# Performance work log

Measured on AMD Instinct MI355X. Metric: run time of the kernel, lower is better.

The kernel has to match this reference:

```python
import jax, jax.numpy as jnp
import numpy as np

# ---- config constants (from ResidualNetConfig) ----
BOUND_LO = jnp.array([-5.0, -5.0, -5.0], dtype=jnp.float32)
BOUND_DIS = jnp.array([10.0, 10.0, 10.0], dtype=jnp.float32)
N_MIN = 200                 # int(ceil(max extent)/resolution) = 10/0.05
PER_LEVEL_SCALE = 2.0
NUM_LEVELS = 4
LOG2_T = 19
T = 1 << LOG2_T
OUTPUT_SDF_SCALE = 0.1
LEAKY_SLOPE = 0.01

# Instant-NGP spatial hash primes (first coord uses 1)
PRIMES = (np.uint32(1), np.uint32(2654435761), np.uint32(805459861))
# 8 corner offsets of the unit cube, [8, 3]
CORNERS = jnp.array([[(c >> d) & 1 for d in range(3)] for c in range(8)], dtype=jnp.uint32)


def hash_grid_encode(xyz01, tables):
    """xyz01: [N,3] in [0,1]; tables: [L,T,F] -> [N, L*F] trilinear hashed features."""
    feats = []
    for l in range(NUM_LEVELS):
        res = jnp.float32(N_MIN * (PER_LEVEL_SCALE ** l))
        pos = xyz01 * res                       # [N,3]
        pfloor = jnp.floor(pos)
        frac = pos - pfloor                     # [N,3]
        base = pfloor.astype(jnp.uint32)        # [N,3]
        corner = base[:, None, :] + CORNERS[None, :, :]   # [N,8,3]
        h = (corner[..., 0] * PRIMES[0]) ^ (corner[..., 1] * PRIMES[1]) ^ (corner[..., 2] * PRIMES[2])
        idx = (h & jnp.uint32(T - 1)).astype(jnp.int32)   # [N,8]
        f = tables[l][idx]                      # [N,8,F] irregular gather
        # trilinear weights: prod over dims of frac (corner=1) or 1-frac (corner=0)
        w = jnp.prod(jnp.where(CORNERS[None].astype(bool), frac[:, None, :], 1.0 - frac[:, None, :]), axis=-1)  # [N,8]
        feats.append(jnp.sum(f * w[..., None], axis=1))   # [N,F]
    return jnp.concatenate(feats, axis=-1)      # [N, L*F]


def leaky_relu(x):
    return jnp.where(x >= 0, x, LEAKY_SLOPE * x)


def setup_inputs() -> dict:
    key = jax.random.key(0)
    k1, k2, k3, k4, k5 = jax.random.split(key, 5)
    N = 2_000_000
    xyz = jax.random.uniform(k1, (N, 3), dtype=jnp.float32) * BOUND_DIS + BOUND_LO
    tables = jax.random.normal(k2, (NUM_LEVELS, T, 2), dtype=jnp.float32) * 1e-2
    W_in = jax.random.normal(k3, (8, 64), dtype=jnp.float32) / np.sqrt(8.0)
    W_h = jax.random.normal(k4, (64, 64), dtype=jnp.float32) / np.sqrt(64.0)
    W_out = jax.random.normal(k5, (64, 1), dtype=jnp.float32) / np.sqrt(64.0)
    return {"xyz": xyz, "tables": tables, "W_in": W_in, "W_h": W_h, "W_out": W_out}


def reference(xyz, tables, W_in, W_h, W_out):
    # scale_with_bound: map xyz into [0,1]^3
    xyz01 = (xyz - BOUND_LO) / BOUND_DIS
    enc = hash_grid_encode(xyz01, tables)        # [N, 8]
    h = leaky_relu(enc @ W_in)                   # hidden layer 1
    h = leaky_relu(h @ W_h)                      # hidden layer 2
    sdf = (h @ W_out).reshape(-1) * OUTPUT_SDF_SCALE
    return sdf
```

## Files before the change

### kernel.cpp

```cpp
#include <hip/hip_runtime.h>
#include <hip/hip_fp16.h>

static constexpr unsigned TSIZE = 1u << 19;
static constexpr unsigned TMASK = TSIZE - 1u;

typedef _Float16 f16;
typedef f16   f16x8 __attribute__((ext_vector_type(8)));
typedef float f32x4 __attribute__((ext_vector_type(4)));

union H2U { __half2 h; unsigned u; };

__global__ __launch_bounds__(256)
void cvt_tables(const float4* __restrict__ in, __half2* __restrict__ out, int n4)
{
    int i = blockIdx.x * 256 + threadIdx.x;
    if (i < n4) {
        float4 v = in[i];
        out[2 * i]     = __floats2half2_rn(v.x, v.y);
        out[2 * i + 1] = __floats2half2_rn(v.z, v.w);
    }
}

__device__ __forceinline__ void hash_level(float px, float py, float pz, int l,
                                           const __half2* __restrict__ tab,
                                           float& e0, float& e1)
{
    const float res = 200.0f * (float)(1 << l);
    const float fx = px * res, fy = py * res, fz = pz * res;
    const float flx = floorf(fx), fly = floorf(fy), flz = floorf(fz);
    const float frx = fx - flx, fry = fy - fly, frz = fz - flz;
    const unsigned bx = (unsigned)flx, by = (unsigned)fly, bz = (unsigned)flz;
    const unsigned hy0 = by * 2654435761u, hy1 = (by + 1u) * 2654435761u;
    const unsigned hz0 = bz * 805459861u,  hz1 = (bz + 1u) * 805459861u;
    const float wx[2] = {1.0f - frx, frx};
    const float wy[2] = {1.0f - fry, fry};
    const float wz[2] = {1.0f - frz, frz};
    e0 = 0.0f; e1 = 0.0f;
    #pragma unroll
    for (int c = 0; c < 8; ++c) {
        unsigned h = (bx + (unsigned)(c & 1))
                   ^ ((c & 2) ? hy1 : hy0)
                   ^ ((c & 4) ? hz1 : hz0);
        __half2 fv = tab[h & TMASK];
        float2 f = __half22float2(fv);
        float w = wx[c & 1] * wy[(c >> 1) & 1] * wz[(c >> 2) & 1];
        e0 = fmaf(f.x, w, e0);
        e1 = fmaf(f.y, w, e1);
    }
}

__device__ __forceinline__ void stage_xyz(const float* __restrict__ xyz, int bbase, int N,
                                          float* sxyz, float& px, float& py, float& pz)
{
    const int g3 = bbase * 3;
    #pragma unroll
    for (int t = 0; t < 3; ++t) {
        int sidx = (int)threadIdx.x + t * 256;
        int g = g3 + sidx;
        sxyz[sidx] = (g < 3 * N) ? __builtin_nontemporal_load(&xyz[g]) : 0.0f;
    }
    __syncthreads();
    px = (sxyz[threadIdx.x * 3 + 0] + 5.0f) * 0.1f;
    py = (sxyz[threadIdx.x * 3 + 1] + 5.0f) * 0.1f;
    pz = (sxyz[threadIdx.x * 3 + 2] + 5.0f) * 0.1f;
}

__global__ __launch_bounds__(256, 8)
void encode01(const float* __restrict__ xyz, const __half2* __restrict__ tab16,
              unsigned long long* __restrict__ enc01, int N)
{
    __shared__ float sxyz[768];
    const int bbase = blockIdx.x * 256;
    const int i = bbase + (int)threadIdx.x;
    float px, py, pz;
    stage_xyz(xyz, bbase, N, sxyz, px, py, pz);

    float e0, e1, e2, e3;
    hash_level(px, py, pz, 0, tab16,         e0, e1);
    hash_level(px, py, pz, 1, tab16 + TSIZE, e2, e3);

    H2U a, b;
    a.h = __floats2half2_rn(e0, e1);
    b.h = __floats2half2_rn(e2, e3);
    if (i < N) {
        unsigned long long v = (unsigned long long)a.u
                             | ((unsigned long long)b.u << 32);
        __builtin_nontemporal_store(v, &enc01[i]);
    }
}

static constexpr int H1_STRIDE = 72;

__global__ __launch_bounds__(256, 2)
void mlp23_mfma(const float* __restrict__ xyz, const __half2* __restrict__ tab16,
                const unsigned long long* __restrict__ enc01,
                const float* __restrict__ Win, const float* __restrict__ Wh,
                const float* __restrict__ Wout, float* __restrict__ out, int N)
{
    __shared__ float sxyz[768];
    __shared__ f16 h1s[256 * H1_STRIDE];

    const int bbase = blockIdx.x * 256;
    const int i = bbase + (int)threadIdx.x;
    float px, py, pz;
    stage_xyz(xyz, bbase, N, sxyz, px, py, pz);

    float enc[8];
    {
        unsigned long long v = __builtin_nontemporal_load(&enc01[i < N ? i : 0]);
        H2U a, b; a.u = (unsigned)v; b.u = (unsigned)(v >> 32);
        float2 f01 = __half22float2(a.h);
        float2 f23 = __half22float2(b.h);
        enc[0] = f01.x; enc[1] = f01.y; enc[2] = f23.x; enc[3] = f23.y;
    }
    hash_level(px, py, pz, 2, tab16 + 2 * TSIZE, enc[4], enc[5]);
    hash_level(px, py, pz, 3, tab16 + 3 * TSIZE, enc[6], enc[7]);

    float h1[64];
    #pragma unroll
    for (int j = 0; j < 64; ++j) h1[j] = 0.0f;
    #pragma unroll
    for (int k = 0; k < 8; ++k) {
        const float e = enc[k];
        #pragma unroll
        for (int j = 0; j < 64; ++j)
            h1[j] = fmaf(e, Win[k * 64 + j], h1[j]);
    }
    {
        f16* row = &h1s[(int)threadIdx.x * H1_STRIDE];
        #pragma unroll
        for (int jj = 0; jj < 8; ++jj) {
            f16x8 v;
            #pragma unroll
            for (int e = 0; e < 8; ++e) {
                float a = h1[jj * 8 + e];
                a = (a >= 0.0f) ? a : 0.01f * a;
                v[e] = (f16)a;
            }
            *(f16x8*)(row + jj * 8) = v;
        }
    }
    __syncthreads();

    const int wave = (int)threadIdx.x >> 6;
    const int lane = (int)threadIdx.x & 63;
    const int c = lane & 15;
    const int q = lane >> 4;
    const f16* wbase = &h1s[wave * 64 * H1_STRIDE];

    f16x8 bfrag[2][4];
    #pragma unroll
    for (int kt = 0; kt < 2; ++kt)
        #pragma unroll
        for (int nt = 0; nt < 4; ++nt)
            #pragma unroll
            for (int j = 0; j < 8; ++j)
                bfrag[kt][nt][j] = (f16)Wh[(kt * 32 + q * 8 + j) * 64 + nt * 16 + c];

    f32x4 Ct[4][4];
    #pragma unroll
    for (int mt = 0; mt < 4; ++mt)
        #pragma unroll
        for (int nt = 0; nt < 4; ++nt)
            Ct[mt][nt] = (f32x4){0.f, 0.f, 0.f, 0.f};

    #pragma unroll
    for (int mt = 0; mt < 4; ++mt) {
        #pragma unroll
        for (int kt = 0; kt < 2; ++kt) {
            const f16x8 a = *(const f16x8*)&wbase[(mt * 16 + c) * H1_STRIDE + kt * 32 + q * 8];
            #pragma unroll
            for (int nt = 0; nt < 4; ++nt)
                Ct[mt][nt] = __builtin_amdgcn_mfma_f32_16x16x32_f16(a, bfrag[kt][nt], Ct[mt][nt], 0, 0, 0);
        }
    }

    float acc3[4][4];
    #pragma unroll
    for (int mt = 0; mt < 4; ++mt)
        #pragma unroll
        for (int r = 0; r < 4; ++r) acc3[mt][r] = 0.0f;

    #pragma unroll
    for (int nt = 0; nt < 4; ++nt) {
        const float wo = Wout[nt * 16 + c];
        #pragma unroll
        for (int mt = 0; mt < 4; ++mt)
            #pragma unroll
            for (int r = 0; r < 4; ++r) {
                float v = Ct[mt][nt][r];
                v = (v >= 0.0f) ? v : 0.01f * v;
                acc3[mt][r] = fmaf(v, wo, acc3[mt][r]);
            }
    }
    #pragma unroll
    for (int mask = 1; mask <= 8; mask <<= 1)
        #pragma unroll
        for (int mt = 0; mt < 4; ++mt)
            #pragma unroll
            for (int r = 0; r < 4; ++r)
                acc3[mt][r] += __shfl_xor(acc3[mt][r], mask, 64);

    if (c == 0) {
        #pragma unroll
        for (int mt = 0; mt < 4; ++mt)
            #pragma unroll
            for (int r = 0; r < 4; ++r) {
                int p = bbase + wave * 64 + mt * 16 + q * 4 + r;
                if (p < N) out[p] = acc3[mt][r] * 0.1f;
            }
    }
}

__global__ __launch_bounds__(256, 2)
void resnet_mono(const float* __restrict__ xyz, const float* __restrict__ tables,
                 const float* __restrict__ Win, const float* __restrict__ Wh,
                 const float* __restrict__ Wout, float* __restrict__ out, int N)
{
    __shared__ float sxyz[768];
    const int bbase = blockIdx.x * 256;
    const int i = bbase + (int)threadIdx.x;
    float px, py, pz;
    stage_xyz(xyz, bbase, N, sxyz, px, py, pz);

    float enc[8];
    #pragma unroll
    for (int l = 0; l < 4; ++l) {
        const float res = 200.0f * (float)(1 << l);
        const float fx = px * res, fy = py * res, fz = pz * res;
        const float flx = floorf(fx), fly = floorf(fy), flz = floorf(fz);
        const float frx = fx - flx, fry = fy - fly, frz = fz - flz;
        const unsigned bx = (unsigned)flx, by = (unsigned)fly, bz = (unsigned)flz;
        const unsigned hy0 = by * 2654435761u, hy1 = (by + 1u) * 2654435761u;
        const unsigned hz0 = bz * 805459861u,  hz1 = (bz + 1u) * 805459861u;
        const float wx[2] = {1.0f - frx, frx};
        const float wy[2] = {1.0f - fry, fry};
        const float wz[2] = {1.0f - frz, frz};
        const float2* tab = (const float2*)tables + (size_t)l * TSIZE;
        float e0 = 0.0f, e1 = 0.0f;
        #pragma unroll
        for (int cc = 0; cc < 8; ++cc) {
            unsigned h = (bx + (unsigned)(cc & 1))
                       ^ ((cc & 2) ? hy1 : hy0)
                       ^ ((cc & 4) ? hz1 : hz0);
            float2 f = tab[h & TMASK];
            float w = wx[cc & 1] * wy[(cc >> 1) & 1] * wz[(cc >> 2) & 1];
            e0 = fmaf(f.x, w, e0);
            e1 = fmaf(f.y, w, e1);
        }
        enc[2 * l] = e0; enc[2 * l + 1] = e1;
    }

    float h1[64];
    #pragma unroll
    for (int j = 0; j < 64; ++j) h1[j] = 0.0f;
    #pragma unroll
    for (int k = 0; k < 8; ++k) {
        const float e = enc[k];
        #pragma unroll
        for (int j = 0; j < 64; ++j)
            h1[j] = fmaf(e, Win[k * 64 + j], h1[j]);
    }
    #pragma unroll
    for (int j = 0; j < 64; ++j)
        h1[j] = (h1[j] >= 0.0f) ? h1[j] : 0.01f * h1[j];

    float sdf = 0.0f;
    #pragma unroll
    for (int j0 = 0; j0 < 64; j0 += 16) {
        float acc[16];
        #pragma unroll
        for (int jj = 0; jj < 16; ++jj) acc[jj] = 0.0f;
        #pragma unroll
        for (int k = 0; k < 64; ++k) {
            const float hk = h1[k];
            #pragma unroll
            for (int jj = 0; jj < 16; ++jj)
                acc[jj] = fmaf(hk, Wh[k * 64 + j0 + jj], acc[jj]);
        }
        #pragma unroll
        for (int jj = 0; jj < 16; ++jj) {
            float a = acc[jj];
            a = (a >= 0.0f) ? a : 0.01f * a;
            sdf = fmaf(a, Wout[j0 + jj], sdf);
        }
    }
    if (i < N) out[i] = sdf * 0.1f;
}

extern "C" void kernel_launch(void* const* d_in, const int* in_sizes, int n_in,
                              void* d_out, int out_size, void* d_ws, size_t ws_size,
                              hipStream_t stream) {
    const float* xyz    = (const float*)d_in[0];
    const float* tables = (const float*)d_in[1];
    const float* Win    = (const float*)d_in[2];
    const float* Wh     = (const float*)d_in[3];
    const float* Wout   = (const float*)d_in[4];
    float* out = (float*)d_out;

    const int N = in_sizes[0] / 3;
    const int blocks = (N + 255) / 256;

    const int tab_floats = in_sizes[1];
    const size_t tab16_bytes = (size_t)tab_floats * 2;
    const size_t enc01_bytes = (size_t)N * 8;

    if (ws_size >= tab16_bytes + enc01_bytes) {
        __half2* tab16 = (__half2*)d_ws;
        unsigned long long* enc01 = (unsigned long long*)((char*)d_ws + tab16_bytes);
        int n4 = tab_floats / 4;
        hipLaunchKernelGGL(cvt_tables, dim3((n4 + 255) / 256), dim3(256), 0, stream,
                           (const float4*)tables, tab16, n4);
        hipLaunchKernelGGL(encode01, dim3(blocks), dim3(256), 0, stream,
                           xyz, tab16, enc01, N);
        hipLaunchKernelGGL(mlp23_mfma, dim3(blocks), dim3(256), 0, stream,
                           xyz, tab16, enc01, Win, Wh, Wout, out, N);
    } else {
        hipLaunchKernelGGL(resnet_mono, dim3(blocks), dim3(256), 0, stream,
                           xyz, tables, Win, Wh, Wout, out, N);
    }
}
```

Baseline: 324.6 us.

## Pair hash-grid corner gathers into 8-byte loads and issue all levels before blending

Within each level, corners c and c+1 differ only in x. When bx is even, their hashed indices (bx^s) and ((bx+1)^s) are adjacent, so one aligned uint2 load fetches both. When bx is odd, four extra single loads fetch the second corner. All gathers for both levels, plus the enc01 load, are now issued before any blending, which exposes memory-level parallelism. Launch bounds change to 4 blocks per SM for both kernels, and the intent is to cut the number of scattered gather instructions and overlap their latency. The cost is more live registers, a divergent branch when bx parity differs across lanes, and occupancy that changes in opposite directions for the two kernels.

Result: no change. 328.7 us (+1.3%).

```diff
diff --git a/kernel.cpp b/kernel.cpp
--- a/kernel.cpp
+++ b/kernel.cpp
@@ -21,31 +21,66 @@
     }
 }
 
-__device__ __forceinline__ void hash_level(float px, float py, float pz, int l,
-                                           const __half2* __restrict__ tab,
-                                           float& e0, float& e1)
-{
+struct HashIssue {
+    uint2    pv[4];
+    unsigned uodd[4];
+    unsigned flags;
+    float    frx, fry, frz;
+};
+
+__device__ __forceinline__ HashIssue hash_issue(float px, float py, float pz, int l,
+                                                const __half2* __restrict__ tab)
+{
+    HashIssue r;
     const float res = 200.0f * (float)(1 << l);
     const float fx = px * res, fy = py * res, fz = pz * res;
     const float flx = floorf(fx), fly = floorf(fy), flz = floorf(fz);
-    const float frx = fx - flx, fry = fy - fly, frz = fz - flz;
+    r.frx = fx - flx; r.fry = fy - fly; r.frz = fz - flz;
     const unsigned bx = (unsigned)flx, by = (unsigned)fly, bz = (unsigned)flz;
     const unsigned hy0 = by * 2654435761u, hy1 = (by + 1u) * 2654435761u;
     const unsigned hz0 = bz * 805459861u,  hz1 = (bz + 1u) * 805459861u;
-    const float wx[2] = {1.0f - frx, frx};
-    const float wy[2] = {1.0f - fry, fry};
-    const float wz[2] = {1.0f - frz, frz};
+    const unsigned syz[4] = { hy0 ^ hz0, hy1 ^ hz0, hy0 ^ hz1, hy1 ^ hz1 };
+    const uint2* __restrict__ tabp = (const uint2*)tab;
+
+    unsigned flags = (bx & 1u) << 4;
+    #pragma unroll
+    for (int p = 0; p < 4; ++p) {
+        const unsigned i0 = (bx ^ syz[p]) & TMASK;
+        r.pv[p] = tabp[i0 >> 1];
+        flags |= (i0 & 1u) << p;
+        r.uodd[p] = 0u;
+    }
+    if (bx & 1u) {
+        #pragma unroll
+        for (int p = 0; p < 4; ++p) {
+            const unsigned i1 = ((bx + 1u) ^ syz[p]) & TMASK;
+            H2U t; t.h = tab[i1];
+            r.uodd[p] = t.u;
+        }
+    }
+    r.flags = flags;
+    return r;
+}
+
+__device__ __forceinline__ void hash_blend(const HashIssue& r, float& e0, float& e1)
+{
+    const float wx0 = 1.0f - r.frx, wx1 = r.frx;
+    const float wyv[2] = {1.0f - r.fry, r.fry};
+    const float wzv[2] = {1.0f - r.frz, r.frz};
+    const bool bxodd = (r.flags >> 4) & 1u;
     e0 = 0.0f; e1 = 0.0f;
     #pragma unroll
-    for (int c = 0; c < 8; ++c) {
-        unsigned h = (bx + (unsigned)(c & 1))
-                   ^ ((c & 2) ? hy1 : hy0)
-                   ^ ((c & 4) ? hz1 : hz0);
-        __half2 fv = tab[h & TMASK];
-        float2 f = __half22float2(fv);
-        float w = wx[c & 1] * wy[(c >> 1) & 1] * wz[(c >> 2) & 1];
-        e0 = fmaf(f.x, w, e0);
-        e1 = fmaf(f.y, w, e1);
+    for (int p = 0; p < 4; ++p) {
+        const bool sw = (r.flags >> p) & 1u;
+        unsigned a = sw ? r.pv[p].y : r.pv[p].x;
+        unsigned b = sw ? r.pv[p].x : r.pv[p].y;
+        b = bxodd ? r.uodd[p] : b;
+        H2U ua, ub; ua.u = a; ub.u = b;
+        const float2 f0 = __half22float2(ua.h);
+        const float2 f1 = __half22float2(ub.h);
+        const float wyz = wyv[p & 1] * wzv[(p >> 1) & 1];
+        e0 = fmaf(fmaf(f1.x, wx1, f0.x * wx0), wyz, e0);
+        e1 = fmaf(fmaf(f1.y, wx1, f0.y * wx0), wyz, e1);
     }
 }
 
@@ -65,7 +100,7 @@
     pz = (sxyz[threadIdx.x * 3 + 2] + 5.0f) * 0.1f;
 }
 
-__global__ __launch_bounds__(256, 8)
+__global__ __launch_bounds__(256, 4)
 void encode01(const float* __restrict__ xyz, const __half2* __restrict__ tab16,
               unsigned long long* __restrict__ enc01, int N)
 {
@@ -75,9 +110,12 @@
     float px, py, pz;
     stage_xyz(xyz, bbase, N, sxyz, px, py, pz);
 
+    HashIssue h0 = hash_issue(px, py, pz, 0, tab16);
+    HashIssue h1 = hash_issue(px, py, pz, 1, tab16 + TSIZE);
+
     float e0, e1, e2, e3;
-    hash_level(px, py, pz, 0, tab16,         e0, e1);
-    hash_level(px, py, pz, 1, tab16 + TSIZE, e2, e3);
+    hash_blend(h0, e0, e1);
+    hash_blend(h1, e2, e3);
 
     H2U a, b;
     a.h = __floats2half2_rn(e0, e1);
@@ -91,7 +129,7 @@
 
 static constexpr int H1_STRIDE = 72;
 
-__global__ __launch_bounds__(256, 2)
+__global__ __launch_bounds__(256, 4)
 void mlp23_mfma(const float* __restrict__ xyz, const __half2* __restrict__ tab16,
                 const unsigned long long* __restrict__ enc01,
                 const float* __restrict__ Win, const float* __restrict__ Wh,
@@ -105,16 +143,19 @@
     float px, py, pz;
     stage_xyz(xyz, bbase, N, sxyz, px, py, pz);
 
+    const unsigned long long v01 = __builtin_nontemporal_load(&enc01[i < N ? i : 0]);
+    HashIssue h2 = hash_issue(px, py, pz, 2, tab16 + 2 * TSIZE);
+    HashIssue h3 = hash_issue(px, py, pz, 3, tab16 + 3 * TSIZE);
+
     float enc[8];
     {
-        unsigned long long v = __builtin_nontemporal_load(&enc01[i < N ? i : 0]);
-        H2U a, b; a.u = (unsigned)v; b.u = (unsigned)(v >> 32);
+        H2U a, b; a.u = (unsigned)v01; b.u = (unsigned)(v01 >> 32);
         float2 f01 = __half22float2(a.h);
         float2 f23 = __half22float2(b.h);
         enc[0] = f01.x; enc[1] = f01.y; enc[2] = f23.x; enc[3] = f23.y;
     }
-    hash_level(px, py, pz, 2, tab16 + 2 * TSIZE, enc[4], enc[5]);
-    hash_level(px, py, pz, 3, tab16 + 3 * TSIZE, enc[6], enc[7]);
+    hash_blend(h2, enc[4], enc[5]);
+    hash_blend(h3, enc[6], enc[7]);
 
     float h1[64];
     #pragma unroll
```
